# Optimization experiments

Hardware: AMD Instinct MI355X
Metric: run time of the kernel (lower is better)

The kernel has to match this reference:

```python
import jax, jax.numpy as jnp
import numpy as np

N_QUBITS = 14
LATENT = 14
DEPTH = 4
BATCH = 256
DIM = 1 << N_QUBITS  # 16384 amplitudes

# PennyLane convention: wire 0 is the most-significant bit of the flat state index.
_idx = np.arange(DIM)
_bits = (_idx[None, :] >> (N_QUBITS - 1 - np.arange(N_QUBITS)[:, None])) & 1  # [n_qubits, DIM]
_parity = np.sum(_bits[:-1] * _bits[1:], axis=0) % 2  # adjacent-pair CZ chain parity
CZ_SIGNS = jnp.asarray(1.0 - 2.0 * _parity, dtype=jnp.complex64)  # [DIM]
Z_SIGNS = jnp.asarray(1 - 2 * _bits[:LATENT], dtype=jnp.float32)  # [LATENT, DIM]


def _rx(t):
    c = jnp.cos(0.5 * t) + 0j
    s = -1j * jnp.sin(0.5 * t)
    m = jnp.stack([jnp.stack([c, s], -1), jnp.stack([s, c], -1)], -2)
    return m.astype(jnp.complex64)


def _ry(t):
    c = jnp.cos(0.5 * t)
    s = jnp.sin(0.5 * t)
    m = jnp.stack([jnp.stack([c, -s], -1), jnp.stack([s, c], -1)], -2)
    return m.astype(jnp.complex64)


def _rz(t):
    e = jnp.exp(-0.5j * t.astype(jnp.complex64))
    z = jnp.zeros_like(e)
    m = jnp.stack([jnp.stack([e, z], -1), jnp.stack([z, jnp.conj(e)], -1)], -2)
    return m.astype(jnp.complex64)


def _apply_1q(state, mat, wire):
    # state: [B, DIM]; mat: [2,2] (shared) or [B,2,2] (per-sample)
    B = state.shape[0]
    left = 1 << wire
    right = 1 << (N_QUBITS - wire - 1)
    st = state.reshape(B, left, 2, right)
    if mat.ndim == 3:
        st = jnp.einsum('bij,bajc->baic', mat, st)
    else:
        st = jnp.einsum('ij,bajc->baic', mat, st)
    return st.reshape(B, DIM)


def setup_inputs() -> dict:
    key = jax.random.key(0)
    k1, k2, k3, k4 = jax.random.split(key, 4)
    conditioning = jax.random.normal(k1, (BATCH, LATENT), dtype=jnp.float32)
    lim = 1.0 / np.sqrt(LATENT)
    W_enc = jax.random.uniform(k2, (N_QUBITS, LATENT), jnp.float32, -lim, lim)
    b_enc = jax.random.uniform(k3, (N_QUBITS,), jnp.float32, -lim, lim)
    # TorchLayer default init: U(0, 2*pi)
    weights = jax.random.uniform(k4, (DEPTH, N_QUBITS, 3), jnp.float32, 0.0, 2.0 * np.pi)
    return {"conditioning": conditioning, "W_enc": W_enc, "b_enc": b_enc, "weights": weights}


def reference(conditioning, W_enc, b_enc, weights):
    # encode: Linear + SiLU -> per-wire rotation angles [B, n_qubits]
    emb = conditioning @ W_enc.T + b_enc
    emb = emb * jax.nn.sigmoid(emb)
    B = emb.shape[0]

    state = jnp.zeros((B, DIM), jnp.complex64).at[:, 0].set(1.0)

    # angle encoding: RX(v) then RY(v) on each wire (per-sample gates)
    for w in range(N_QUBITS):
        v = emb[:, w]
        U = jnp.einsum('bij,bjk->bik', _ry(v), _rx(v))  # [B,2,2]
        state = _apply_1q(state, U, w)

    # variational layers: RZ, RX, RY per wire (shared gates), then CZ chain
    for d in range(DEPTH):
        for w in range(N_QUBITS):
            p = weights[d, w]
            U = _ry(p[2]) @ _rx(p[1]) @ _rz(p[0])  # [2,2]
            state = _apply_1q(state, U, w)
        state = state * CZ_SIGNS  # all adjacent CZs fused into one diagonal

    probs = state.real ** 2 + state.imag ** 2  # [B, DIM]
    latent = probs @ Z_SIGNS.T  # <Z_w> for w in range(LATENT) -> [B, LATENT]

    # F.layer_norm over last dim, no affine params
    mu = jnp.mean(latent, axis=-1, keepdims=True)
    var = jnp.var(latent, axis=-1, keepdims=True)
    return (latent - mu) / jnp.sqrt(var + 1e-5)
```

## Files before the change

### kernel.cpp

```cpp
#include <hip/hip_runtime.h>
#include <math.h>

#define NQ    14
#define DIM   16384
#define DEPTH 4

typedef __attribute__((ext_vector_type(2))) float f2;
typedef __attribute__((ext_vector_type(4))) float f4;

__device__ __forceinline__ f2 cmul(f2 a, f2 b) {
    return (f2){a.x*b.x - a.y*b.y, a.x*b.y + a.y*b.x};
}
__device__ __forceinline__ f2 cmac2(f2 x, f2 u, f2 us, f2 y, f2 v, f2 vs) {
    f2 r = x.xx * u;
    r += x.yy * us;
    r += y.xx * v;
    r += y.yy * vs;
    return r;
}


template<int CTRL>
__device__ __forceinline__ f2 dpp2(f2 v) {
    union U { f2 f; int i[2]; } u, r;
    u.f = v;
    r.i[0] = __builtin_amdgcn_update_dpp(0, u.i[0], CTRL, 0xF, 0xF, true);
    r.i[1] = __builtin_amdgcn_update_dpp(0, u.i[1], CTRL, 0xF, 0xF, true);
    return r.f;
}
template<int XB> __device__ __forceinline__ f2 lxchg(f2 v);
template<> __device__ __forceinline__ f2 lxchg<1>(f2 v) { return dpp2<0xB1>(v); }
template<> __device__ __forceinline__ f2 lxchg<2>(f2 v) { return dpp2<0x4E>(v); }
template<> __device__ __forceinline__ f2 lxchg<8>(f2 v) { return dpp2<0x128>(v); }

template<int MASK>
__device__ __forceinline__ void reg_gate(f2 a[16], const f4* __restrict__ G) {
    f4 g0 = G[0], g1 = G[1], g2 = G[2], g3 = G[3];
    #pragma unroll
    for (int l = 0; l < 16; ++l) {
        if (l & MASK) continue;
        const int j = l | MASK;
        f2 x = a[l], y = a[j];
        a[l] = cmac2(x, g0.xy, g0.zw, y, g1.xy, g1.zw);
        a[j] = cmac2(x, g2.xy, g2.zw, y, g3.xy, g3.zw);
    }
}

template<int XB>
__device__ __forceinline__ void lane_gate(f2 a[16], const f4* __restrict__ G, int t) {
    const bool hi = (t & XB) != 0;
    f4 c1 = G[hi ? 3 : 0];
    f4 c2 = G[hi ? 2 : 1];
    #pragma unroll
    for (int l = 0; l < 16; ++l) {
        f2 p = lxchg<XB>(a[l]);
        a[l] = cmac2(a[l], c1.xy, c1.zw, p, c2.xy, c2.zw);
    }
}

__device__ __forceinline__ void cz_A(f2 a[16], int t) {
    const int n = t & 63, w = t >> 6;
    const int pT = (__popc(w & (w >> 1)) + __popc(n & (n >> 1)) + ((n & 1) & (w >> 3))) & 1;
    const float F0 = pT ? -1.f : 1.f;
    const float F1 = (pT ^ ((n >> 5) & 1)) ? -1.f : 1.f;
    #pragma unroll
    for (int l = 0; l < 16; ++l) {
        float s = (l & 1) ? F1 : F0;
        if (__popc(l & (l >> 1)) & 1) s = -s;
        a[l] *= s;
    }
}

__device__ __forceinline__ void cz_B(f2 a[16], int t) {
    const int n = t & 63, w = t >> 6;
    const int n0 = n & 1, n1 = (n >> 1) & 1, n2 = (n >> 2) & 1;
    const int n3 = (n >> 3) & 1, n4 = (n >> 4) & 1, n5 = (n >> 5) & 1;
    const int pT = ((n2 & n4) ^ (n4 & n0) ^ (n0 & n5) ^ (n5 & n1) ^ (n1 & n3)
                    ^ (n3 & (w & 1)) ^ (__popc(w & (w >> 1)) & 1));
    const float F0 = pT ? -1.f : 1.f;
    const float F1 = (pT ^ n2) ? -1.f : 1.f;
    #pragma unroll
    for (int l = 0; l < 16; ++l) {
        float s = (l & 8) ? F1 : F0;
        if (__popc(l & (l >> 1)) & 1) s = -s;
        a[l] *= s;
    }
}

__global__ void qlg_prep(const float* __restrict__ wts,
                         f4* __restrict__ G)
{
    const int t = threadIdx.x;
    if (t >= DEPTH * NQ) return;
    const int d = t / NQ, ww = t % NQ;
    const float p0 = wts[(d*NQ + ww)*3 + 0];
    const float p1 = wts[(d*NQ + ww)*3 + 1];
    const float p2 = wts[(d*NQ + ww)*3 + 2];
    float s0, c0, s1, c1, s2, c2;
    sincosf(0.5f*p0, &s0, &c0);
    sincosf(0.5f*p1, &s1, &c1);
    sincosf(0.5f*p2, &s2, &c2);
    f2 e0  = (f2){c0, -s0};
    f2 e0c = (f2){c0,  s0};
    f2 is1 = (f2){0.f, -s1};
    f2 m00 = c1 * e0;
    f2 m01 = cmul(is1, e0c);
    f2 m10 = cmul(is1, e0);
    f2 m11 = c1 * e0c;
    f2 u00 = c2*m00 - s2*m10;
    f2 u01 = c2*m01 - s2*m11;
    f2 u10 = s2*m00 + c2*m10;
    f2 u11 = s2*m01 + c2*m11;
    if (d == 0) {
        G[168 + ww*2 + 0] = (f4){u00.x, u00.y, u01.x, u01.y};
        G[168 + ww*2 + 1] = (f4){u10.x, u10.y, u11.x, u11.y};
    } else {
        const bool isA = (ww <= 3) || (ww == 6) || (ww == 8) || (ww == 9);
        int slot;
        if (isA) slot = (ww <= 3) ? ww : (ww == 6 ? 4 : (ww == 8 ? 5 : 6));
        else     slot = (ww >= 10) ? (ww - 10) : (ww == 4 ? 4 : (ww == 5 ? 5 : 6));
        const int h = (d == 1) ? (isA ? 0 : 1)
                    : (d == 2) ? (isA ? 3 : 2)
                               : (isA ? 4 : 5);
        const int base = (h*7 + slot)*4;
        G[base + 0] = (f4){u00.x, u00.y, -u00.y, u00.x};
        G[base + 1] = (f4){u01.x, u01.y, -u01.y, u01.x};
        G[base + 2] = (f4){u10.x, u10.y, -u10.y, u10.x};
        G[base + 3] = (f4){u11.x, u11.y, -u11.y, u11.x};
    }
}

__global__ __launch_bounds__(1024)
void qlg_kernel(const float* __restrict__ cond,
                const float* __restrict__ Wenc,
                const float* __restrict__ benc,
                const f4* __restrict__ gG,
                float* __restrict__ out)
{
    __shared__ f2 st[DIM];
    __shared__ f2 qv[NQ][2];
    __shared__ f2 Phi[128];
    __shared__ f2 Plo[128];
    __shared__ float embS[NQ];
    __shared__ float wred[16][NQ];
    __shared__ float lat[NQ];

    const int b = blockIdx.x;
    const int t = threadIdx.x;
    const int n = t & 63, w = t >> 6;
    const int bB = (w << 10)
                 | (((n >> 3) & 1) << 5) | (((n >> 1) & 1) << 4)
                 | (((n >> 5) & 1) << 3) | ((n & 1) << 2)
                 | (((n >> 4) & 1) << 1) | ((n >> 2) & 1);

    if (t < NQ) {
        float s = benc[t];
        #pragma unroll
        for (int k = 0; k < NQ; ++k) s += cond[b*NQ + k] * Wenc[t*NQ + k];
        float e = s / (1.0f + __expf(-s));
        embS[t] = e;
    }
    __syncthreads();

    if (t < NQ) {
        float v = embS[t];
        float s, c;
        sincosf(0.5f*v, &s, &c);
        f2 a0 = (f2){c*c,  s*s};
        f2 a1 = (f2){s*c, -s*c};
        f4 va = gG[168 + t*2], vb = gG[168 + t*2 + 1];
        f2 u00 = (f2){va.x, va.y}, u01 = (f2){va.z, va.w};
        f2 u10 = (f2){vb.x, vb.y}, u11 = (f2){vb.z, vb.w};
        qv[t][0] = cmul(u00, a0) + cmul(u01, a1);
        qv[t][1] = cmul(u10, a0) + cmul(u11, a1);
    }
    __syncthreads();

    if (t < 128) {
        f2 p = qv[0][(t >> 6) & 1];
        #pragma unroll
        for (int ww = 1; ww <= 6; ++ww) p = cmul(p, qv[ww][(t >> (6 - ww)) & 1]);
        Phi[t] = p;
    } else if (t < 256) {
        const int j = t - 128;
        f2 p = qv[7][(j >> 6) & 1];
        #pragma unroll
        for (int ww = 8; ww <= 13; ++ww) p = cmul(p, qv[ww][(j >> (13 - ww)) & 1]);
        Plo[j] = p;
    }
    __syncthreads();

    f2 a[16];
    {
        f2 plo = Plo[((n & 7) << 4) | w];
        #pragma unroll
        for (int l = 0; l < 16; ++l)
            a[l] = cmul(Phi[(l << 3) | (n >> 3)], plo);
        cz_A(a, t);
    }

    #pragma unroll
    for (int h = 0; h < 6; ++h) {
        const f4* __restrict__ g = gG + h*7*4;
        reg_gate<8>(a, g + 0*4);
        reg_gate<4>(a, g + 1*4);
        reg_gate<2>(a, g + 2*4);
        reg_gate<1>(a, g + 3*4);
        lane_gate<8>(a, g + 4*4, t);
        lane_gate<2>(a, g + 5*4, t);
        lane_gate<1>(a, g + 6*4, t);
        if (h == 1)      cz_B(a, t);
        else if (h == 3) cz_A(a, t);
        if (h == 0 || h == 4) {
            #pragma unroll
            for (int l = 0; l < 16; ++l) st[t + (l << 10)] = a[l];
            __syncthreads();
            #pragma unroll
            for (int l = 0; l < 16; ++l) a[l] = st[bB + (l << 6)];
        } else if (h == 2) {
            #pragma unroll
            for (int l = 0; l < 16; ++l) st[bB + (l << 6)] = a[l];
            __syncthreads();
            #pragma unroll
            for (int l = 0; l < 16; ++l) a[l] = st[t + (l << 10)];
        }
    }

    float SU, Q10, Q11, Q12, Q13;
    {
        SU = Q10 = Q11 = Q12 = Q13 = 0.f;
        #pragma unroll
        for (int l = 0; l < 16; ++l) {
            float p = a[l].x*a[l].x + a[l].y*a[l].y;
            SU  += p;
            Q10 += (l & 8) ? -p : p;
            Q11 += (l & 4) ? -p : p;
            Q12 += (l & 2) ? -p : p;
            Q13 += (l & 1) ? -p : p;
        }
    }

    {
        const int lane = t & 63, wv = t >> 6;
        const int sbit[10] = {9, 8, 7, 6, 3, 1, 5, 0, 4, 2};
        #pragma unroll
        for (int ww = 0; ww < NQ; ++ww) {
            float v;
            if      (ww == 10) v = Q10;
            else if (ww == 11) v = Q11;
            else if (ww == 12) v = Q12;
            else if (ww == 13) v = Q13;
            else               v = ((t >> sbit[ww]) & 1) ? -SU : SU;
            #pragma unroll
            for (int off = 32; off > 0; off >>= 1) v += __shfl_down(v, off, 64);
            if (lane == 0) wred[wv][ww] = v;
        }
    }
    __syncthreads();
    if (t < NQ) {
        float s = 0.f;
        #pragma unroll
        for (int k = 0; k < 16; ++k) s += wred[k][t];
        lat[t] = s;
    }
    __syncthreads();
    if (t < NQ) {
        float mu = 0.f;
        #pragma unroll
        for (int k = 0; k < NQ; ++k) mu += lat[k];
        mu *= (1.0f / NQ);
        float var = 0.f;
        #pragma unroll
        for (int k = 0; k < NQ; ++k) { float dv = lat[k] - mu; var += dv*dv; }
        var *= (1.0f / NQ);
        out[b*NQ + t] = (lat[t] - mu) * rsqrtf(var + 1e-5f);
    }
}

extern "C" void kernel_launch(void* const* d_in, const int* in_sizes, int n_in,
                              void* d_out, int out_size, void* d_ws, size_t ws_size,
                              hipStream_t stream)
{
    (void)n_in; (void)ws_size; (void)out_size;
    const float* cond = (const float*)d_in[0];
    const float* Wenc = (const float*)d_in[1];
    const float* benc = (const float*)d_in[2];
    const float* wts  = (const float*)d_in[3];
    float* out = (float*)d_out;
    f4* G = (f4*)d_ws;
    const int B = in_sizes[0] / NQ;
    qlg_prep<<<dim3(1), dim3(64), 0, stream>>>(wts, G);
    qlg_kernel<<<dim3(B), dim3(1024), 0, stream>>>(cond, Wenc, benc, G, out);
}
```

Baseline: 93.70 us.

## Simulate state vector in packed fp16 half2 with split real/imag planes

Stores the amplitudes as packed half2 registers, with real and imaginary parts in separate planes, and applies the gates with packed fp16 FMAs. The qubit held in the low/high halves is handled by a pair gate that swaps the two halves, and the CZ signs become sign-bit XOR masks. The shared-memory transpose buffer is halved, and each lane exchange moves one DPP word instead of two. This aims to double arithmetic throughput and cut LDS traffic, at the risk of fp16 rounding error building up over about 56 gates.

```diff
diff --git a/kernel.cpp b/kernel.cpp
--- a/kernel.cpp
+++ b/kernel.cpp
@@ -1,4 +1,5 @@
 #include <hip/hip_runtime.h>
+#include <hip/hip_fp16.h>
 #include <math.h>
 
 #define NQ    14
@@ -7,88 +8,114 @@
 
 typedef __attribute__((ext_vector_type(2))) float f2;
 typedef __attribute__((ext_vector_type(4))) float f4;
+typedef __half2 h2;
 
 __device__ __forceinline__ f2 cmul(f2 a, f2 b) {
     return (f2){a.x*b.x - a.y*b.y, a.x*b.y + a.y*b.x};
 }
-__device__ __forceinline__ f2 cmac2(f2 x, f2 u, f2 us, f2 y, f2 v, f2 vs) {
-    f2 r = x.xx * u;
-    r += x.yy * us;
-    r += y.xx * v;
-    r += y.yy * vs;
-    return r;
-}
-
+__device__ __forceinline__ float czsgn(int e) {
+    return (__popc(e & (e >> 1)) & 1) ? -1.0f : 1.0f;
+}
+
+
+__device__ __forceinline__ void cfma2(h2 c1r, h2 c1i, h2 c2r, h2 c2i,
+                                      h2 xr, h2 xi, h2 yr, h2 yi,
+                                      h2& or_, h2& oi_)
+{
+    or_ = __hfma2(c1r, xr, __hfma2(__hneg2(c1i), xi,
+          __hfma2(c2r, yr, __hmul2(__hneg2(c2i), yi))));
+    oi_ = __hfma2(c1r, xi, __hfma2(c1i, xr,
+          __hfma2(c2r, yi, __hmul2(c2i, yr))));
+}
+
+__device__ __forceinline__ h2 hxor(h2 v, unsigned m) {
+    union { h2 h; unsigned u; } x; x.h = v; x.u ^= m; return x.h;
+}
 
 template<int CTRL>
-__device__ __forceinline__ f2 dpp2(f2 v) {
-    union U { f2 f; int i[2]; } u, r;
-    u.f = v;
-    r.i[0] = __builtin_amdgcn_update_dpp(0, u.i[0], CTRL, 0xF, 0xF, true);
-    r.i[1] = __builtin_amdgcn_update_dpp(0, u.i[1], CTRL, 0xF, 0xF, true);
-    return r.f;
-}
-template<int XB> __device__ __forceinline__ f2 lxchg(f2 v);
-template<> __device__ __forceinline__ f2 lxchg<1>(f2 v) { return dpp2<0xB1>(v); }
-template<> __device__ __forceinline__ f2 lxchg<2>(f2 v) { return dpp2<0x4E>(v); }
-template<> __device__ __forceinline__ f2 lxchg<8>(f2 v) { return dpp2<0x128>(v); }
-
-template<int MASK>
-__device__ __forceinline__ void reg_gate(f2 a[16], const f4* __restrict__ G) {
-    f4 g0 = G[0], g1 = G[1], g2 = G[2], g3 = G[3];
-    #pragma unroll
-    for (int l = 0; l < 16; ++l) {
-        if (l & MASK) continue;
-        const int j = l | MASK;
-        f2 x = a[l], y = a[j];
-        a[l] = cmac2(x, g0.xy, g0.zw, y, g1.xy, g1.zw);
-        a[j] = cmac2(x, g2.xy, g2.zw, y, g3.xy, g3.zw);
+__device__ __forceinline__ h2 dpph(h2 v) {
+    union { h2 h; int i; } u, r;
+    u.h = v;
+    r.i = __builtin_amdgcn_update_dpp(0, u.i, CTRL, 0xF, 0xF, true);
+    return r.h;
+}
+template<int XB> __device__ __forceinline__ h2 lx2(h2 v);
+template<> __device__ __forceinline__ h2 lx2<1>(h2 v) { return dpph<0xB1>(v); }
+template<> __device__ __forceinline__ h2 lx2<2>(h2 v) { return dpph<0x4E>(v); }
+template<> __device__ __forceinline__ h2 lx2<8>(h2 v) { return dpph<0x128>(v); }
+
+template<int KM>
+__device__ __forceinline__ void reg_gate_h(h2 hr[8], h2 hi[8], const h2* __restrict__ g) {
+    h2 c00r = g[0], c00i = g[1], c01r = g[2], c01i = g[3];
+    h2 c10r = g[4], c10i = g[5], c11r = g[6], c11i = g[7];
+    #pragma unroll
+    for (int k = 0; k < 8; ++k) {
+        if (k & KM) continue;
+        const int j = k | KM;
+        h2 xr = hr[k], xi = hi[k], yr = hr[j], yi = hi[j];
+        cfma2(c00r, c00i, c01r, c01i, xr, xi, yr, yi, hr[k], hi[k]);
+        cfma2(c10r, c10i, c11r, c11i, xr, xi, yr, yi, hr[j], hi[j]);
+    }
+}
+
+__device__ __forceinline__ void pair_gate_h(h2 hr[8], h2 hi[8], const h2* __restrict__ g) {
+    h2 Ar = g[0], Ai = g[1], Br = g[2], Bi = g[3];
+    #pragma unroll
+    for (int k = 0; k < 8; ++k) {
+        h2 pr = __lowhigh2highlow(hr[k]);
+        h2 pi = __lowhigh2highlow(hi[k]);
+        cfma2(Ar, Ai, Br, Bi, hr[k], hi[k], pr, pi, hr[k], hi[k]);
     }
 }
 
 template<int XB>
-__device__ __forceinline__ void lane_gate(f2 a[16], const f4* __restrict__ G, int t) {
-    const bool hi = (t & XB) != 0;
-    f4 c1 = G[hi ? 3 : 0];
-    f4 c2 = G[hi ? 2 : 1];
-    #pragma unroll
-    for (int l = 0; l < 16; ++l) {
-        f2 p = lxchg<XB>(a[l]);
-        a[l] = cmac2(a[l], c1.xy, c1.zw, p, c2.xy, c2.zw);
-    }
-}
-
-__device__ __forceinline__ void cz_A(f2 a[16], int t) {
+__device__ __forceinline__ void lane_gate_h(h2 hr[8], h2 hi[8], const h2* __restrict__ g, int t) {
+    const bool hiL = (t & XB) != 0;
+    h2 c1r = hiL ? g[6] : g[0];
+    h2 c1i = hiL ? g[7] : g[1];
+    h2 c2r = hiL ? g[4] : g[2];
+    h2 c2i = hiL ? g[5] : g[3];
+    #pragma unroll
+    for (int k = 0; k < 8; ++k) {
+        h2 pr = lx2<XB>(hr[k]);
+        h2 pi = lx2<XB>(hi[k]);
+        cfma2(c1r, c1i, c2r, c2i, hr[k], hi[k], pr, pi, hr[k], hi[k]);
+    }
+}
+
+__device__ __forceinline__ void cz_A_h(h2 hr[8], h2 hi[8], int t) {
     const int n = t & 63, w = t >> 6;
     const int pT = (__popc(w & (w >> 1)) + __popc(n & (n >> 1)) + ((n & 1) & (w >> 3))) & 1;
-    const float F0 = pT ? -1.f : 1.f;
-    const float F1 = (pT ^ ((n >> 5) & 1)) ? -1.f : 1.f;
-    #pragma unroll
-    for (int l = 0; l < 16; ++l) {
-        float s = (l & 1) ? F1 : F0;
-        if (__popc(l & (l >> 1)) & 1) s = -s;
-        a[l] *= s;
-    }
-}
-
-__device__ __forceinline__ void cz_B(f2 a[16], int t) {
+    const int f0 = pT, f1 = pT ^ ((n >> 5) & 1);
+    #pragma unroll
+    for (int k = 0; k < 8; ++k) {
+        const int stlo = __popc((2*k) & ((2*k) >> 1)) & 1;
+        const int sthi = __popc((2*k+1) & ((2*k+1) >> 1)) & 1;
+        const unsigned mask = ((f0 ^ stlo) ? 0x8000u : 0u)
+                            | ((f1 ^ sthi) ? 0x80000000u : 0u);
+        hr[k] = hxor(hr[k], mask); hi[k] = hxor(hi[k], mask);
+    }
+}
+__device__ __forceinline__ void cz_B_h(h2 hr[8], h2 hi[8], int t) {
     const int n = t & 63, w = t >> 6;
     const int n0 = n & 1, n1 = (n >> 1) & 1, n2 = (n >> 2) & 1;
     const int n3 = (n >> 3) & 1, n4 = (n >> 4) & 1, n5 = (n >> 5) & 1;
     const int pT = ((n2 & n4) ^ (n4 & n0) ^ (n0 & n5) ^ (n5 & n1) ^ (n1 & n3)
                     ^ (n3 & (w & 1)) ^ (__popc(w & (w >> 1)) & 1));
-    const float F0 = pT ? -1.f : 1.f;
-    const float F1 = (pT ^ n2) ? -1.f : 1.f;
-    #pragma unroll
-    for (int l = 0; l < 16; ++l) {
-        float s = (l & 8) ? F1 : F0;
-        if (__popc(l & (l >> 1)) & 1) s = -s;
-        a[l] *= s;
-    }
-}
-
-__global__ void qlg_prep(const float* __restrict__ wts,
-                         f4* __restrict__ G)
+    const int f0 = pT, f1 = pT ^ n2;
+    #pragma unroll
+    for (int k = 0; k < 8; ++k) {
+        const int fs = (k & 4) ? f1 : f0;
+        const int stlo = __popc((2*k) & ((2*k) >> 1)) & 1;
+        const int sthi = __popc((2*k+1) & ((2*k+1) >> 1)) & 1;
+        const unsigned mask = ((fs ^ stlo) ? 0x8000u : 0u)
+                            | ((fs ^ sthi) ? 0x80000000u : 0u);
+        hr[k] = hxor(hr[k], mask); hi[k] = hxor(hi[k], mask);
+    }
+}
+
+__global__ void qlg_prep(const float* __restrict__ wts, h2* __restrict__ Gh,
+                         f4* __restrict__ G0)
 {
     const int t = threadIdx.x;
     if (t >= DEPTH * NQ) return;
@@ -112,21 +139,29 @@
     f2 u10 = s2*m00 + c2*m10;
     f2 u11 = s2*m01 + c2*m11;
     if (d == 0) {
-        G[168 + ww*2 + 0] = (f4){u00.x, u00.y, u01.x, u01.y};
-        G[168 + ww*2 + 1] = (f4){u10.x, u10.y, u11.x, u11.y};
+        G0[ww*2 + 0] = (f4){u00.x, u00.y, u01.x, u01.y};
+        G0[ww*2 + 1] = (f4){u10.x, u10.y, u11.x, u11.y};
+        return;
+    }
+    const bool isA = (ww <= 3) || (ww == 6) || (ww == 8) || (ww == 9);
+    int slot;
+    if (isA) slot = (ww <= 3) ? ww : (ww == 6 ? 4 : (ww == 8 ? 5 : 6));
+    else     slot = (ww >= 10) ? (ww - 10) : (ww == 4 ? 4 : (ww == 5 ? 5 : 6));
+    const int h = (d == 1) ? (isA ? 0 : 1)
+                : (d == 2) ? (isA ? 3 : 2)
+                           : (isA ? 4 : 5);
+    h2* g = Gh + (h*7 + slot)*8;
+    if (slot == 3) {
+        g[0] = __halves2half2(__float2half_rn(u00.x), __float2half_rn(u11.x));
+        g[1] = __halves2half2(__float2half_rn(u00.y), __float2half_rn(u11.y));
+        g[2] = __halves2half2(__float2half_rn(u01.x), __float2half_rn(u10.x));
+        g[3] = __halves2half2(__float2half_rn(u01.y), __float2half_rn(u10.y));
+        g[4] = g[5] = g[6] = g[7] = __float2half2_rn(0.f);
     } else {
-        const bool isA = (ww <= 3) || (ww == 6) || (ww == 8) || (ww == 9);
-        int slot;
-        if (isA) slot = (ww <= 3) ? ww : (ww == 6 ? 4 : (ww == 8 ? 5 : 6));
-        else     slot = (ww >= 10) ? (ww - 10) : (ww == 4 ? 4 : (ww == 5 ? 5 : 6));
-        const int h = (d == 1) ? (isA ? 0 : 1)
-                    : (d == 2) ? (isA ? 3 : 2)
-                               : (isA ? 4 : 5);
-        const int base = (h*7 + slot)*4;
-        G[base + 0] = (f4){u00.x, u00.y, -u00.y, u00.x};
-        G[base + 1] = (f4){u01.x, u01.y, -u01.y, u01.x};
-        G[base + 2] = (f4){u10.x, u10.y, -u10.y, u10.x};
-        G[base + 3] = (f4){u11.x, u11.y, -u11.y, u11.x};
+        g[0] = __float2half2_rn(u00.x); g[1] = __float2half2_rn(u00.y);
+        g[2] = __float2half2_rn(u01.x); g[3] = __float2half2_rn(u01.y);
+        g[4] = __float2half2_rn(u10.x); g[5] = __float2half2_rn(u10.y);
+        g[6] = __float2half2_rn(u11.x); g[7] = __float2half2_rn(u11.y);
     }
 }
 
@@ -134,10 +169,11 @@
 void qlg_kernel(const float* __restrict__ cond,
                 const float* __restrict__ Wenc,
                 const float* __restrict__ benc,
-                const f4* __restrict__ gG,
+                const h2* __restrict__ Gh,
+                const f4* __restrict__ G0,
                 float* __restrict__ out)
 {
-    __shared__ f2 st[DIM];
+    __shared__ h2 st[DIM];
     __shared__ f2 qv[NQ][2];
     __shared__ f2 Phi[128];
     __shared__ f2 Plo[128];
@@ -157,8 +193,7 @@
         float s = benc[t];
         #pragma unroll
         for (int k = 0; k < NQ; ++k) s += cond[b*NQ + k] * Wenc[t*NQ + k];
-        float e = s / (1.0f + __expf(-s));
-        embS[t] = e;
+        embS[t] = s / (1.0f + __expf(-s));
     }
     __syncthreads();
 
@@ -168,7 +203,7 @@
         sincosf(0.5f*v, &s, &c);
         f2 a0 = (f2){c*c,  s*s};
         f2 a1 = (f2){s*c, -s*c};
-        f4 va = gG[168 + t*2], vb = gG[168 + t*2 + 1];
+        f4 va = G0[t*2], vb = G0[t*2 + 1];
         f2 u00 = (f2){va.x, va.y}, u01 = (f2){va.z, va.w};
         f2 u10 = (f2){vb.x, vb.y}, u11 = (f2){vb.z, vb.w};
         qv[t][0] = cmul(u00, a0) + cmul(u01, a1);
@@ -190,39 +225,61 @@
     }
     __syncthreads();
 
-    f2 a[16];
+    h2 hr[8], hi[8];
     {
         f2 plo = Plo[((n & 7) << 4) | w];
         #pragma unroll
-        for (int l = 0; l < 16; ++l)
-            a[l] = cmul(Phi[(l << 3) | (n >> 3)], plo);
-        cz_A(a, t);
+        for (int k = 0; k < 8; ++k) {
+            const int l0 = 2*k, l1 = 2*k + 1;
+            const int e0 = (l0 << 10) | (n << 4) | w;
+            const int e1 = (l1 << 10) | (n << 4) | w;
+            f2 a0 = cmul(Phi[(l0 << 3) | (n >> 3)], plo) * czsgn(e0);
+            f2 a1 = cmul(Phi[(l1 << 3) | (n >> 3)], plo) * czsgn(e1);
+            hr[k] = __floats2half2_rn(a0.x, a1.x);
+            hi[k] = __floats2half2_rn(a0.y, a1.y);
+        }
     }
 
     #pragma unroll
     for (int h = 0; h < 6; ++h) {
-        const f4* __restrict__ g = gG + h*7*4;
-        reg_gate<8>(a, g + 0*4);
-        reg_gate<4>(a, g + 1*4);
-        reg_gate<2>(a, g + 2*4);
-        reg_gate<1>(a, g + 3*4);
-        lane_gate<8>(a, g + 4*4, t);
-        lane_gate<2>(a, g + 5*4, t);
-        lane_gate<1>(a, g + 6*4, t);
-        if (h == 1)      cz_B(a, t);
-        else if (h == 3) cz_A(a, t);
+        const h2* __restrict__ g = Gh + h*7*8;
+        reg_gate_h<4>(hr, hi, g + 0*8);
+        reg_gate_h<2>(hr, hi, g + 1*8);
+        reg_gate_h<1>(hr, hi, g + 2*8);
+        pair_gate_h(hr, hi, g + 3*8);
+        lane_gate_h<8>(hr, hi, g + 4*8, t);
+        lane_gate_h<2>(hr, hi, g + 5*8, t);
+        lane_gate_h<1>(hr, hi, g + 6*8, t);
+        if (h == 1)      cz_B_h(hr, hi, t);
+        else if (h == 3) cz_A_h(hr, hi, t);
         if (h == 0 || h == 4) {
             #pragma unroll
-            for (int l = 0; l < 16; ++l) st[t + (l << 10)] = a[l];
+            for (int k = 0; k < 8; ++k) {
+                st[t + ((2*k)   << 10)] = __halves2half2(__low2half(hr[k]),  __low2half(hi[k]));
+                st[t + ((2*k+1) << 10)] = __halves2half2(__high2half(hr[k]), __high2half(hi[k]));
+            }
             __syncthreads();
             #pragma unroll
-            for (int l = 0; l < 16; ++l) a[l] = st[bB + (l << 6)];
+            for (int k = 0; k < 8; ++k) {
+                h2 w0 = st[bB + ((2*k)   << 6)];
+                h2 w1 = st[bB + ((2*k+1) << 6)];
+                hr[k] = __halves2half2(__low2half(w0),  __low2half(w1));
+                hi[k] = __halves2half2(__high2half(w0), __high2half(w1));
+            }
         } else if (h == 2) {
             #pragma unroll
-            for (int l = 0; l < 16; ++l) st[bB + (l << 6)] = a[l];
+            for (int k = 0; k < 8; ++k) {
+                st[bB + ((2*k)   << 6)] = __halves2half2(__low2half(hr[k]),  __low2half(hi[k]));
+                st[bB + ((2*k+1) << 6)] = __halves2half2(__high2half(hr[k]), __high2half(hi[k]));
+            }
             __syncthreads();
             #pragma unroll
-            for (int l = 0; l < 16; ++l) a[l] = st[t + (l << 10)];
+            for (int k = 0; k < 8; ++k) {
+                h2 w0 = st[t + ((2*k)   << 10)];
+                h2 w1 = st[t + ((2*k+1) << 10)];
+                hr[k] = __halves2half2(__low2half(w0),  __low2half(w1));
+                hi[k] = __halves2half2(__high2half(w0), __high2half(w1));
+            }
         }
     }
 
@@ -230,13 +287,17 @@
     {
         SU = Q10 = Q11 = Q12 = Q13 = 0.f;
         #pragma unroll
-        for (int l = 0; l < 16; ++l) {
-            float p = a[l].x*a[l].x + a[l].y*a[l].y;
-            SU  += p;
-            Q10 += (l & 8) ? -p : p;
-            Q11 += (l & 4) ? -p : p;
-            Q12 += (l & 2) ? -p : p;
-            Q13 += (l & 1) ? -p : p;
+        for (int k = 0; k < 8; ++k) {
+            float2 fr = __half22float2(hr[k]);
+            float2 fi = __half22float2(hi[k]);
+            float pl = fr.x*fr.x + fi.x*fi.x;
+            float ph = fr.y*fr.y + fi.y*fi.y;
+            float g2 = pl + ph;
+            SU  += g2;
+            Q13 += pl - ph;
+            Q10 += (k & 4) ? -g2 : g2;
+            Q11 += (k & 2) ? -g2 : g2;
+            Q12 += (k & 1) ? -g2 : g2;
         }
     }
 
@@ -287,8 +348,9 @@
     const float* benc = (const float*)d_in[2];
     const float* wts  = (const float*)d_in[3];
     float* out = (float*)d_out;
-    f4* G = (f4*)d_ws;
+    h2* Gh = (h2*)d_ws;
+    f4* G0 = (f4*)((char*)d_ws + 2048);
     const int B = in_sizes[0] / NQ;
-    qlg_prep<<<dim3(1), dim3(64), 0, stream>>>(wts, G);
-    qlg_kernel<<<dim3(B), dim3(1024), 0, stream>>>(cond, Wenc, benc, G, out);
-}
+    qlg_prep<<<dim3(1), dim3(64), 0, stream>>>(wts, Gh, G0);
+    qlg_kernel<<<dim3(B), dim3(1024), 0, stream>>>(cond, Wenc, benc, Gh, G0, out);
+}
```

After: 91.91 us. About the same (-1.9%).
